# Performance work log

Hardware: AMD Instinct MI355X
Metric: run time of the kernel (lower is better)

## Reference

```python
import jax, jax.numpy as jnp
import numpy as np

B, SEQ, DIM = 4, 2048, 2048
NH, HD = 16, 128            # head_dim = dim // n_head
HID = 5632                  # int(2*(4*dim)/3) rounded up to multiple_of=256
EPS = 1e-5
THETA = 500000.0


def setup_inputs() -> dict:
    key = jax.random.key(0)
    ks = jax.random.split(key, 9)
    s = 0.02  # init scale keeps activations/logits well-conditioned
    x = jax.random.normal(ks[0], (B, SEQ, DIM), jnp.float32)
    wq = jax.random.normal(ks[1], (DIM, DIM), jnp.float32) * s
    wk = jax.random.normal(ks[2], (DIM, DIM), jnp.float32) * s
    wv = jax.random.normal(ks[3], (DIM, DIM), jnp.float32) * s
    wo = jax.random.normal(ks[4], (DIM, DIM), jnp.float32) * s
    w1 = jax.random.normal(ks[5], (DIM, HID), jnp.float32) * s
    w2 = jax.random.normal(ks[6], (HID, DIM), jnp.float32) * s
    w3 = jax.random.normal(ks[7], (DIM, HID), jnp.float32) * s
    attn_norm_w = jnp.ones((DIM,), jnp.float32)
    ffn_norm_w = jnp.ones((DIM,), jnp.float32)
    # RoPE tables (real/imag of freqs_cis), [seq, head_dim//2]
    inv = 1.0 / (THETA ** (jnp.arange(0, HD, 2, dtype=jnp.float32) / HD))
    ang = jnp.arange(SEQ, dtype=jnp.float32)[:, None] * inv[None, :]
    return dict(x=x, wq=wq, wk=wk, wv=wv, wo=wo, w1=w1, w2=w2, w3=w3,
                attn_norm_w=attn_norm_w, ffn_norm_w=ffn_norm_w,
                freqs_cos=jnp.cos(ang), freqs_sin=jnp.sin(ang))


def rmsnorm(x, w, eps=EPS):
    return x * jax.lax.rsqrt(jnp.mean(x * x, axis=-1, keepdims=True) + eps) * w


def rope(x, cos, sin):
    # x: [b, s, h, d]; pairs (d0,d1),(d2,d3),... treated as complex, multiplied by e^{i*ang}
    a, b = x[..., 0::2], x[..., 1::2]
    c = cos[None, :, None, :]
    s = sin[None, :, None, :]
    return jnp.stack([a * c - b * s, a * s + b * c], axis=-1).reshape(x.shape)


def block(x, wq, wk, wv, wo, w1, w2, w3, attn_norm_w, ffn_norm_w, freqs_cos, freqs_sin):
    b, s, d = x.shape
    # --- attention sublayer ---
    hn = rmsnorm(x, attn_norm_w)
    q = (hn @ wq).reshape(b, s, NH, HD)
    k = (hn @ wk).reshape(b, s, NH, HD)
    v = (hn @ wv).reshape(b, s, NH, HD)
    q = rope(q, freqs_cos, freqs_sin)
    k = rope(k, freqs_cos, freqs_sin)
    scores = jnp.einsum('bqhd,bkhd->bhqk', q, k) / np.float32(np.sqrt(HD))
    mask = jnp.triu(jnp.full((s, s), -jnp.inf, dtype=scores.dtype), k=1)
    p = jax.nn.softmax(scores + mask, axis=-1)
    attn = jnp.einsum('bhqk,bkhd->bqhd', p, v).reshape(b, s, d) @ wo
    h = x + attn
    # --- SwiGLU FFN sublayer ---
    fn = rmsnorm(h, ffn_norm_w)
    ffn = (jax.nn.silu(fn @ w1) * (fn @ w3)) @ w2
    return h + ffn


def reference(x, wq, wk, wv, wo, w1, w2, w3, attn_norm_w, ffn_norm_w, freqs_cos, freqs_sin):
    return block(x, wq, wk, wv, wo, w1, w2, w3, attn_norm_w, ffn_norm_w, freqs_cos, freqs_sin)
```

## Files before the change

### kernel.cpp

```cpp
#include <hip/hip_runtime.h>
#include <stdint.h>

#define DIMV 2048
#define SEQV 2048
#define NHV 16
#define HDV 128
#define HIDV 5632
#define NROWS 8192
#define LDP 6144

typedef short bf16x8 __attribute__((ext_vector_type(8)));
typedef float f32x4 __attribute__((ext_vector_type(4)));
typedef unsigned short u16x8 __attribute__((ext_vector_type(8)));

#define GLD16(src, dst) __builtin_amdgcn_global_load_lds( \
    (const __attribute__((address_space(1))) unsigned int*)(src), \
    (__attribute__((address_space(3))) unsigned int*)(dst), 16, 0, 0)

__device__ __forceinline__ float bf2f(unsigned short u){
  union { unsigned u; float f; } x; x.u = ((unsigned)u) << 16; return x.f;
}
__device__ __forceinline__ unsigned short f2bf(float f){
  union { float f; unsigned u; } x; x.f = f;
  unsigned r = x.u + 0x7fffu + ((x.u >> 16) & 1u);
  return (unsigned short)(r >> 16);
}

__global__ void transpose_cast4(const float* s0, const float* s1, const float* s2, const float* s3,
                                unsigned short* d0g, unsigned short* d1g, unsigned short* d2g, unsigned short* d3g,
                                int R, int C){
  __shared__ alignas(16) unsigned short tile[32][33];
  const float* in; unsigned short* out;
  switch (blockIdx.z){
    case 0: in = s0; out = d0g; break;
    case 1: in = s1; out = d1g; break;
    case 2: in = s2; out = d2g; break;
    default: in = s3; out = d3g; break;
  }
  int c0 = blockIdx.x * 32, r0 = blockIdx.y * 32;
  int tx = threadIdx.x, ty = threadIdx.y;
#pragma unroll
  for (int i = 0; i < 32; i += 8)
    tile[ty + i][tx] = f2bf(in[(long)(r0 + ty + i) * C + (c0 + tx)]);
  __syncthreads();
#pragma unroll
  for (int i = 0; i < 32; i += 8)
    out[(long)(c0 + ty + i) * R + (r0 + tx)] = tile[tx][ty + i];
}

__global__ void transpose_v(const unsigned short* __restrict__ packed, unsigned short* __restrict__ vt){
  __shared__ alignas(16) unsigned short tile[32][33];
  int bh = blockIdx.z;
  int b = bh >> 4, h = bh & 15;
  int d0 = blockIdx.y * 32, s0 = blockIdx.x * 32;
  int tx = threadIdx.x, ty = threadIdx.y;
  const unsigned short* src = packed + (long)b * SEQV * LDP + 4096 + (long)h * HDV;
  unsigned short* dst = vt + (long)bh * HDV * SEQV;
#pragma unroll
  for (int i = 0; i < 32; i += 8)
    tile[ty + i][tx] = src[(long)(s0 + ty + i) * LDP + d0 + tx];
  __syncthreads();
#pragma unroll
  for (int i = 0; i < 32; i += 8)
    dst[(long)(d0 + ty + i) * SEQV + s0 + tx] = tile[tx][ty + i];
}

__global__ __launch_bounds__(256) void rmsnorm_k(const float* __restrict__ x,
                                                 const float* __restrict__ w,
                                                 unsigned short* __restrict__ out){
  int row = blockIdx.x, t = threadIdx.x;
  const float* xr = x + (long)row * DIMV;
  float4 v0 = ((const float4*)xr)[t * 2];
  float4 v1 = ((const float4*)xr)[t * 2 + 1];
  float ss = v0.x*v0.x + v0.y*v0.y + v0.z*v0.z + v0.w*v0.w
           + v1.x*v1.x + v1.y*v1.y + v1.z*v1.z + v1.w*v1.w;
#pragma unroll
  for (int off = 32; off; off >>= 1) ss += __shfl_down(ss, off);
  __shared__ float red[4];
  if ((t & 63) == 0) red[t >> 6] = ss;
  __syncthreads();
  float tot = red[0] + red[1] + red[2] + red[3];
  float sc = rsqrtf(tot * (1.0f / DIMV) + 1e-5f);
  const float* wr = w + t * 8;
  float vv[8] = {v0.x, v0.y, v0.z, v0.w, v1.x, v1.y, v1.z, v1.w};
  u16x8 o;
#pragma unroll
  for (int e = 0; e < 8; e++) o[e] = f2bf(vv[e] * sc * wr[e]);
  *(u16x8*)(out + (long)row * DIMV + t * 8) = o;
}

#define SCHEDB() __builtin_amdgcn_sched_barrier(0)
#define SBAR()   __builtin_amdgcn_s_barrier()

template <int MODE>
__global__ __launch_bounds__(512, 2) void gemm256(const unsigned short* __restrict__ A, int lda,
                                                  const unsigned short* __restrict__ Bt,
                                                  unsigned short* __restrict__ Cb,
                                                  float* __restrict__ Cf,
                                                  const float* __restrict__ resid,
                                                  int ldc, int M, int N, int K){
  __shared__ alignas(16) unsigned short As[2][256 * 64];
  __shared__ alignas(16) unsigned short Bs[2][256 * 64];
  int m0 = blockIdx.y * 256, n0 = blockIdx.x * 256;
  int tid = threadIdx.x, w = tid >> 6, l = tid & 63;
  int wm = w >> 2, wn = w & 3;
  int l15 = l & 15, l4 = l >> 4;
  int sr8 = l >> 3, sl = l & 7;
  int nt = K / 64;

  f32x4 acc[8][4];
#pragma unroll
  for (int i = 0; i < 8; i++)
#pragma unroll
    for (int j = 0; j < 4; j++) acc[i][j] = (f32x4){0.f, 0.f, 0.f, 0.f};

#define GSTAGE(Gp, ld_, r0_, slab) { \
    _Pragma("unroll") \
    for (int r = 0; r < 2; r++){ \
      int row = (r * 8 + w) * 8 + sr8; \
      int cs = sl ^ (row & 7); \
      GLD16((Gp) + (long)((r0_) + row) * (ld_) + cs * 8, (slab) + (r * 8 + w) * 512); \
    } }
#define STAGE_A(tt, half) { int _t = (tt); if (_t < nt) GSTAGE(A + _t * 64, lda, m0 + (half) * 128, &As[_t & 1][(half) * 8192]) }
#define STAGE_B(tt, half) { int _t = (tt); if (_t < nt) GSTAGE(Bt + _t * 64, K, n0 + (half) * 128, &Bs[_t & 1][(half) * 8192]) }
#define LDA8(mi, ks) (*(const bf16x8*)(&As[bi][(wm * 128 + (mi) * 16 + l15) * 64 + (((ks) * 4 + l4) ^ (l15 & 7)) * 8]))
#define LDB8(ni, ks) (*(const bf16x8*)(&Bs[bi][(wn * 64 + (ni) * 16 + l15) * 64 + (((ks) * 4 + l4) ^ (l15 & 7)) * 8]))
#define MFMA4x2(AF, BF, MOFF, NOFF) { \
    _Pragma("unroll") \
    for (int mi = 0; mi < 4; mi++) \
      _Pragma("unroll") \
      for (int ni = 0; ni < 2; ni++) \
        _Pragma("unroll") \
        for (int ks = 0; ks < 2; ks++) \
          acc[mi + (MOFF)][ni + (NOFF)] = __builtin_amdgcn_mfma_f32_16x16x32_bf16(AF[mi][ks], BF[ni][ks], acc[mi + (MOFF)][ni + (NOFF)], 0, 0, 0); }

  STAGE_A(0, 0); STAGE_A(0, 1); STAGE_B(0, 0); STAGE_B(0, 1);
  STAGE_A(1, 0); STAGE_A(1, 1);
  asm volatile("s_waitcnt vmcnt(4)" ::: "memory");
  __syncthreads();

  for (int t = 0; t < nt; t++){
    int bi = t & 1;
    bf16x8 a03[4][2], a47[4][2], b01[2][2], b23[2][2];
#pragma unroll
    for (int mi = 0; mi < 4; mi++){ a03[mi][0] = LDA8(mi, 0); a03[mi][1] = LDA8(mi, 1); }
#pragma unroll
    for (int ni = 0; ni < 2; ni++){ b01[ni][0] = LDB8(ni, 0); b01[ni][1] = LDB8(ni, 1); }
    STAGE_B(t + 1, 0);
    SBAR();
    asm volatile("s_waitcnt lgkmcnt(0)" ::: "memory");
    SCHEDB();
    __builtin_amdgcn_s_setprio(1);
    MFMA4x2(a03, b01, 0, 0);
    __builtin_amdgcn_s_setprio(0);
    SBAR();
#pragma unroll
    for (int mi = 0; mi < 4; mi++){ a47[mi][0] = LDA8(mi + 4, 0); a47[mi][1] = LDA8(mi + 4, 1); }
    STAGE_B(t + 1, 1);
    SBAR();
    asm volatile("s_waitcnt lgkmcnt(0)" ::: "memory");
    SCHEDB();
    __builtin_amdgcn_s_setprio(1);
    MFMA4x2(a47, b01, 4, 0);
    __builtin_amdgcn_s_setprio(0);
    SBAR();
#pragma unroll
    for (int ni = 0; ni < 2; ni++){ b23[ni][0] = LDB8(ni + 2, 0); b23[ni][1] = LDB8(ni + 2, 1); }
    STAGE_A(t + 2, 0);
    SBAR();
    asm volatile("s_waitcnt lgkmcnt(0)" ::: "memory");
    SCHEDB();
    __builtin_amdgcn_s_setprio(1);
    MFMA4x2(a03, b23, 0, 2);
    __builtin_amdgcn_s_setprio(0);
    SBAR();
    STAGE_A(t + 2, 1);
    SBAR();
    __builtin_amdgcn_s_setprio(1);
    MFMA4x2(a47, b23, 4, 2);
    __builtin_amdgcn_s_setprio(0);
    if (t + 2 < nt) asm volatile("s_waitcnt vmcnt(4)" ::: "memory");
    else            asm volatile("s_waitcnt vmcnt(0)" ::: "memory");
    SBAR();
  }
#undef GSTAGE
#undef STAGE_A
#undef STAGE_B
#undef LDA8
#undef LDB8
#undef MFMA4x2

#pragma unroll
  for (int mi = 0; mi < 8; mi++)
#pragma unroll
    for (int ni = 0; ni < 4; ni++)
#pragma unroll
      for (int r = 0; r < 4; r++){
        int row = m0 + wm * 128 + mi * 16 + l4 * 4 + r;
        int col = n0 + wn * 64 + ni * 16 + l15;
        long idx = (long)row * ldc + col;
        float v = acc[mi][ni][r];
        if (MODE == 0) Cb[idx] = f2bf(v);
        else           Cf[idx] = v + resid[idx];
      }
}

__global__ __launch_bounds__(512, 2) void ffn13_256(const unsigned short* __restrict__ A,
                                                    const unsigned short* __restrict__ B1t,
                                                    const unsigned short* __restrict__ B3t,
                                                    unsigned short* __restrict__ G,
                                                    int M, int N, int K){
  __shared__ alignas(16) unsigned short As[2][256 * 64];
  __shared__ alignas(16) unsigned short B1s[2][128 * 64];
  __shared__ alignas(16) unsigned short B3s[2][128 * 64];
  int m0 = blockIdx.y * 256, n0 = blockIdx.x * 128;
  int tid = threadIdx.x, w = tid >> 6, l = tid & 63;
  int wm = w >> 2, wn = w & 3;
  int l15 = l & 15, l4 = l >> 4;
  int sr8 = l >> 3, sl = l & 7;
  int nt = K / 64;

  f32x4 acc1[8][2], acc3[8][2];
#pragma unroll
  for (int i = 0; i < 8; i++)
#pragma unroll
    for (int j = 0; j < 2; j++){ acc1[i][j] = (f32x4){0.f,0.f,0.f,0.f}; acc3[i][j] = (f32x4){0.f,0.f,0.f,0.f}; }

#define GSTAGE(Gp, ld_, r0_, slab) { \
    _Pragma("unroll") \
    for (int r = 0; r < 2; r++){ \
      int row = (r * 8 + w) * 8 + sr8; \
      int cs = sl ^ (row & 7); \
      GLD16((Gp) + (long)((r0_) + row) * (ld_) + cs * 8, (slab) + (r * 8 + w) * 512); \
    } }
#define STAGE_A(tt, half) { int _t = (tt); if (_t < nt) GSTAGE(A + _t * 64, K, m0 + (half) * 128, &As[_t & 1][(half) * 8192]) }
#define STAGE_B1(tt) { int _t = (tt); if (_t < nt) GSTAGE(B1t + _t * 64, K, n0, &B1s[_t & 1][0]) }
#define STAGE_B3(tt) { int _t = (tt); if (_t < nt) GSTAGE(B3t + _t * 64, K, n0, &B3s[_t & 1][0]) }
#define LDA8(mi, ks) (*(const bf16x8*)(&As[bi][(wm * 128 + (mi) * 16 + l15) * 64 + (((ks) * 4 + l4) ^ (l15 & 7)) * 8]))
#define LDB18(ni, ks) (*(const bf16x8*)(&B1s[bi][(wn * 32 + (ni) * 16 + l15) * 64 + (((ks) * 4 + l4) ^ (l15 & 7)) * 8]))
#define LDB38(ni, ks) (*(const bf16x8*)(&B3s[bi][(wn * 32 + (ni) * 16 + l15) * 64 + (((ks) * 4 + l4) ^ (l15 & 7)) * 8]))
#define MFMA4x2(AF, BF, ACC, MOFF) { \
    _Pragma("unroll") \
    for (int mi = 0; mi < 4; mi++) \
      _Pragma("unroll") \
      for (int ni = 0; ni < 2; ni++) \
        _Pragma("unroll") \
        for (int ks = 0; ks < 2; ks++) \
          ACC[mi + (MOFF)][ni] = __builtin_amdgcn_mfma_f32_16x16x32_bf16(AF[mi][ks], BF[ni][ks], ACC[mi + (MOFF)][ni], 0, 0, 0); }

  STAGE_A(0, 0); STAGE_A(0, 1); STAGE_B1(0); STAGE_B3(0);
  STAGE_A(1, 0); STAGE_A(1, 1);
  asm volatile("s_waitcnt vmcnt(4)" ::: "memory");
  __syncthreads();

  for (int t = 0; t < nt; t++){
    int bi = t & 1;
    bf16x8 a03[4][2], a47[4][2], b1f[2][2], b3f[2][2];
#pragma unroll
    for (int mi = 0; mi < 4; mi++){ a03[mi][0] = LDA8(mi, 0); a03[mi][1] = LDA8(mi, 1); }
#pragma unroll
    for (int ni = 0; ni < 2; ni++){ b1f[ni][0] = LDB18(ni, 0); b1f[ni][1] = LDB18(ni, 1); }
    STAGE_B1(t + 1);
    SBAR();
    asm volatile("s_waitcnt lgkmcnt(0)" ::: "memory");
    SCHEDB();
    __builtin_amdgcn_s_setprio(1);
    MFMA4x2(a03, b1f, acc1, 0);
    __builtin_amdgcn_s_setprio(0);
    SBAR();
#pragma unroll
    for (int mi = 0; mi < 4; mi++){ a47[mi][0] = LDA8(mi + 4, 0); a47[mi][1] = LDA8(mi + 4, 1); }
    STAGE_B3(t + 1);
    SBAR();
    asm volatile("s_waitcnt lgkmcnt(0)" ::: "memory");
    SCHEDB();
    __builtin_amdgcn_s_setprio(1);
    MFMA4x2(a47, b1f, acc1, 4);
    __builtin_amdgcn_s_setprio(0);
    SBAR();
#pragma unroll
    for (int ni = 0; ni < 2; ni++){ b3f[ni][0] = LDB38(ni, 0); b3f[ni][1] = LDB38(ni, 1); }
    STAGE_A(t + 2, 0);
    SBAR();
    asm volatile("s_waitcnt lgkmcnt(0)" ::: "memory");
    SCHEDB();
    __builtin_amdgcn_s_setprio(1);
    MFMA4x2(a03, b3f, acc3, 0);
    __builtin_amdgcn_s_setprio(0);
    SBAR();
    STAGE_A(t + 2, 1);
    SBAR();
    __builtin_amdgcn_s_setprio(1);
    MFMA4x2(a47, b3f, acc3, 4);
    __builtin_amdgcn_s_setprio(0);
    if (t + 2 < nt) asm volatile("s_waitcnt vmcnt(4)" ::: "memory");
    else            asm volatile("s_waitcnt vmcnt(0)" ::: "memory");
    SBAR();
  }
#undef GSTAGE
#undef STAGE_A
#undef STAGE_B1
#undef STAGE_B3
#undef LDA8
#undef LDB18
#undef LDB38
#undef MFMA4x2

#pragma unroll
  for (int mi = 0; mi < 8; mi++)
#pragma unroll
    for (int ni = 0; ni < 2; ni++)
#pragma unroll
      for (int r = 0; r < 4; r++){
        int row = m0 + wm * 128 + mi * 16 + l4 * 4 + r;
        int col = n0 + wn * 32 + ni * 16 + l15;
        float a = acc1[mi][ni][r];
        float si = a * (1.f / (1.f + __expf(-a)));
        G[(long)row * N + col] = f2bf(si * acc3[mi][ni][r]);
      }
}

__global__ __launch_bounds__(256) void rope_k(unsigned short* __restrict__ p,
                                              const float* __restrict__ cosT,
                                              const float* __restrict__ sinT,
                                              float qscale){
  long idx = (long)blockIdx.x * 256 + threadIdx.x;
  int i = (int)(idx & 63);
  long t = idx >> 6;
  int h = (int)(t & 15);
  long row = t >> 4;
  int s = (int)(row & (SEQV - 1));
  float c = cosT[s * 64 + i], sn = sinT[s * 64 + i];
  long base = row * LDP + h * HDV + 2 * i;
  unsigned pq = *(unsigned*)(p + base);
  float a = bf2f((unsigned short)(pq & 0xffff)), b = bf2f((unsigned short)(pq >> 16));
  float ra = (a * c - b * sn) * qscale, rb = (a * sn + b * c) * qscale;
  *(unsigned*)(p + base) = (unsigned)f2bf(ra) | ((unsigned)f2bf(rb) << 16);
  unsigned pk = *(unsigned*)(p + base + 2048);
  a = bf2f((unsigned short)(pk & 0xffff)); b = bf2f((unsigned short)(pk >> 16));
  ra = a * c - b * sn; rb = a * sn + b * c;
  *(unsigned*)(p + base + 2048) = (unsigned)f2bf(ra) | ((unsigned)f2bf(rb) << 16);
}

__global__ __launch_bounds__(512) void attn_k(unsigned short* __restrict__ p,
                                              const unsigned short* __restrict__ vt){
  __shared__ alignas(16) unsigned short Ks[2][64 * 128];
  __shared__ alignas(16) unsigned short Vs[2][128 * 64];
  __shared__ alignas(16) unsigned short Ps[8][16 * 64];
  int qt = (gridDim.x - 1) - blockIdx.x;
  int bh = blockIdx.y;
  int b = bh >> 4, h = bh & 15;
  int tid = threadIdx.x, w = tid >> 6, l = tid & 63;
  int l15 = l & 15, l4 = l >> 4;
  int qrow0 = qt * 128 + w * 16;
  long baseQ = (long)b * SEQV * LDP + (long)h * HDV;
  long baseV = (long)bh * HDV * SEQV;

  bf16x8 qf[4];
#pragma unroll
  for (int dc = 0; dc < 4; dc++)
    qf[dc] = *(const bf16x8*)(p + baseQ + (long)(qrow0 + l15) * LDP + dc * 32 + l4 * 8);

  f32x4 acc[8];
#pragma unroll
  for (int df = 0; df < 8; df++) acc[df] = (f32x4){0.f, 0.f, 0.f, 0.f};
  float mOld[4], lsum[4];
#pragma unroll
  for (int r = 0; r < 4; r++){ mOld[r] = -1e30f; lsum[r] = 0.f; }

#define ATTN_STAGE(buf, kt) {                                                       \
    int k0 = (kt) * 64;                                                             \
    _Pragma("unroll")                                                               \
    for (int i = 0; i < 2; i++){                                                    \
      int row = w * 8 + i * 4 + (l >> 4);                                           \
      int slot = (l & 15) ^ (row & 7);                                              \
      GLD16(p + baseQ + 2048 + (long)(k0 + row) * LDP + slot * 8,                   \
            Ks[buf] + (w * 8 + i * 4) * 128);                                       \
    }                                                                               \
    _Pragma("unroll")                                                               \
    for (int i = 0; i < 2; i++){                                                    \
      int row = w * 16 + i * 8 + (l >> 3);                                          \
      int slot = (l & 7) ^ (row & 7);                                               \
      GLD16(vt + baseV + (long)row * SEQV + k0 + slot * 8,                          \
            Vs[buf] + (w * 16 + i * 8) * 64);                                       \
    } }

  int ntile = 2 * (qt + 1);
  ATTN_STAGE(0, 0);
  asm volatile("s_waitcnt vmcnt(0)" ::: "memory");
  __syncthreads();
  int cur = 0;
  for (int tki = 0; tki < ntile; tki++){
    int k0 = tki * 64;
    if (tki + 1 < ntile) ATTN_STAGE(cur ^ 1, tki + 1);

    float s[4][4];
    __builtin_amdgcn_s_setprio(1);
#pragma unroll
    for (int kf = 0; kf < 4; kf++){
      f32x4 sf = (f32x4){0.f, 0.f, 0.f, 0.f};
#pragma unroll
      for (int dc = 0; dc < 4; dc++){
        bf16x8 kb = *(const bf16x8*)(Ks[cur] + (kf * 16 + l15) * 128 + (((dc * 4 + l4) ^ (l15 & 7)) * 8));
        sf = __builtin_amdgcn_mfma_f32_16x16x32_bf16(qf[dc], kb, sf, 0, 0, 0);
      }
      int key = k0 + kf * 16 + l15;
#pragma unroll
      for (int r = 0; r < 4; r++){
        int rowi = qrow0 + l4 * 4 + r;
        s[kf][r] = (key <= rowi) ? sf[r] : -1e30f;
      }
    }
    __builtin_amdgcn_s_setprio(0);
    float scale[4];
#pragma unroll
    for (int r = 0; r < 4; r++){
      float vmax = fmaxf(fmaxf(s[0][r], s[1][r]), fmaxf(s[2][r], s[3][r]));
      for (int mm = 8; mm; mm >>= 1) vmax = fmaxf(vmax, __shfl_xor(vmax, mm));
      float mNew = fmaxf(mOld[r], vmax);
      scale[r] = __expf(mOld[r] - mNew);
      float ps = 0.f;
#pragma unroll
      for (int kf = 0; kf < 4; kf++){
        float pp = __expf(s[kf][r] - mNew);
        s[kf][r] = pp;
        ps += pp;
      }
      for (int mm = 8; mm; mm >>= 1) ps += __shfl_xor(ps, mm);
      lsum[r] = lsum[r] * scale[r] + ps;
      mOld[r] = mNew;
    }
#pragma unroll
    for (int df = 0; df < 8; df++)
#pragma unroll
      for (int r = 0; r < 4; r++) acc[df][r] *= scale[r];
#pragma unroll
    for (int kf = 0; kf < 4; kf++)
#pragma unroll
      for (int r = 0; r < 4; r++){
        int row = l4 * 4 + r;
        int sidx = row * 64 + (((((kf * 16 + l15) * 2)) ^ ((row & 7) << 4)) >> 1);
        Ps[w][sidx] = f2bf(s[kf][r]);
      }
    __builtin_amdgcn_s_setprio(1);
#pragma unroll
    for (int kc = 0; kc < 2; kc++){
      bf16x8 pa = *(const bf16x8*)(Ps[w] + l15 * 64 + (((kc * 64 + l4 * 16) ^ ((l15 & 7) << 4)) >> 1));
#pragma unroll
      for (int df = 0; df < 8; df++){
        bf16x8 vb = *(const bf16x8*)(Vs[cur] + (df * 16 + l15) * 64 + (((kc * 4 + l4) ^ (l15 & 7)) * 8));
        acc[df] = __builtin_amdgcn_mfma_f32_16x16x32_bf16(pa, vb, acc[df], 0, 0, 0);
      }
    }
    __builtin_amdgcn_s_setprio(0);
    asm volatile("s_waitcnt vmcnt(0)" ::: "memory");
    __syncthreads();
    cur ^= 1;
  }
#pragma unroll
  for (int df = 0; df < 8; df++)
#pragma unroll
    for (int r = 0; r < 4; r++){
      int rows = qrow0 + l4 * 4 + r;
      p[baseQ + (long)rows * LDP + df * 16 + l15] = f2bf(acc[df][r] / lsum[r]);
    }
#undef ATTN_STAGE
}

extern "C" void kernel_launch(void* const* d_in, const int* in_sizes, int n_in,
                              void* d_out, int out_size, void* d_ws, size_t ws_size,
                              hipStream_t stream){
  const float* x    = (const float*)d_in[0];
  const float* wq   = (const float*)d_in[1];
  const float* wk   = (const float*)d_in[2];
  const float* wv   = (const float*)d_in[3];
  const float* wo   = (const float*)d_in[4];
  const float* w1   = (const float*)d_in[5];
  const float* w2   = (const float*)d_in[6];
  const float* w3   = (const float*)d_in[7];
  const float* anw  = (const float*)d_in[8];
  const float* fnw  = (const float*)d_in[9];
  const float* fcos = (const float*)d_in[10];
  const float* fsin = (const float*)d_in[11];

  char* ws = (char*)d_ws;
  size_t off = 0;
  auto alloc = [&](size_t bytes) -> void* {
    void* p = ws + off;
    off += (bytes + 255) & ~(size_t)255;
    return p;
  };
  const size_t SQ = (size_t)DIMV * DIMV * 2;
  const size_t SW = (size_t)DIMV * HIDV * 2;
  const size_t SA = (size_t)NROWS * DIMV * 2;
  const size_t SP = (size_t)NROWS * LDP * 2;

  unsigned short* wqT = (unsigned short*)alloc(SQ);
  unsigned short* wkT = (unsigned short*)alloc(SQ);
  unsigned short* wvT = (unsigned short*)alloc(SQ);
  unsigned short* woT = (unsigned short*)alloc(SQ);
  unsigned short* w1T = (unsigned short*)alloc(SW);
  unsigned short* w3T = (unsigned short*)alloc(SW);
  unsigned short* w2T = (unsigned short*)alloc(SW);
  unsigned short* hn  = (unsigned short*)alloc(SA);
  unsigned short* pk  = (unsigned short*)alloc(SP);
  unsigned short* vtb = hn;
  unsigned short* g   = pk;
  float* hf = (float*)d_out;
  (void)ws_size; (void)in_sizes; (void)n_in; (void)out_size;
  (void)wkT; (void)wvT;

  dim3 tb(32, 8);
  transpose_cast4<<<dim3(DIMV/32, DIMV/32, 4), tb, 0, stream>>>(wq, wk, wv, wo, wqT, wkT, wvT, woT, DIMV, DIMV);
  transpose_cast4<<<dim3(HIDV/32, DIMV/32, 2), tb, 0, stream>>>(w1, w3, nullptr, nullptr, w1T, w3T, nullptr, nullptr, DIMV, HIDV);
  transpose_cast4<<<dim3(DIMV/32, HIDV/32, 1), tb, 0, stream>>>(w2, nullptr, nullptr, nullptr, w2T, nullptr, nullptr, nullptr, HIDV, DIMV);

  rmsnorm_k<<<NROWS, 256, 0, stream>>>(x, anw, hn);

  gemm256<0><<<dim3(LDP/256, NROWS/256), 512, 0, stream>>>(hn, DIMV, wqT, pk, nullptr, nullptr, LDP, NROWS, LDP, DIMV);

  rope_k<<<(NROWS * NHV * 64) / 256, 256, 0, stream>>>(pk, fcos, fsin, 0.08838834764831845f);

  transpose_v<<<dim3(SEQV/32, HDV/32, 4 * NHV), tb, 0, stream>>>(pk, vtb);

  attn_k<<<dim3(SEQV/128, 4 * NHV), 512, 0, stream>>>(pk, vtb);

  gemm256<1><<<dim3(DIMV/256, NROWS/256), 512, 0, stream>>>(pk, LDP, woT, nullptr, hf, x, DIMV, NROWS, DIMV, DIMV);

  rmsnorm_k<<<NROWS, 256, 0, stream>>>(hf, fnw, hn);

  ffn13_256<<<dim3(HIDV/128, NROWS/256), 512, 0, stream>>>(hn, w1T, w3T, g, NROWS, HIDV, DIMV);

  gemm256<1><<<dim3(DIMV/256, NROWS/256), 512, 0, stream>>>(g, HIDV, w2T, nullptr, hf, (const float*)hf, DIMV, NROWS, DIMV, HIDV);
}
```

Before: 1.253 ms.

## Switch GEMM and FFN13 kernels from 16x16x32 to 32x32x16 bf16 MFMA tiles

Replaces the 16x16x32 MFMA instructions in both the generic 256x256 GEMM and the fused w1/w3 SwiGLU kernel with 32x32x16 MFMAs. LDS fragment loads, accumulator layout (f32x16) and the epilogue row/column mapping are rewritten to match the larger tile. Bigger MFMA tiles need fewer LDS fragment reads per FLOP and issue fewer instructions. The cost is a different swizzle access pattern that may cause LDS bank conflicts, and the same register pressure.

```diff
diff --git a/kernel.cpp b/kernel.cpp
--- a/kernel.cpp
+++ b/kernel.cpp
@@ -11,6 +11,7 @@
 
 typedef short bf16x8 __attribute__((ext_vector_type(8)));
 typedef float f32x4 __attribute__((ext_vector_type(4)));
+typedef float f32x16 __attribute__((ext_vector_type(16)));
 typedef unsigned short u16x8 __attribute__((ext_vector_type(8)));
 
 #define GLD16(src, dst) __builtin_amdgcn_global_load_lds( \
@@ -104,15 +105,17 @@
   int m0 = blockIdx.y * 256, n0 = blockIdx.x * 256;
   int tid = threadIdx.x, w = tid >> 6, l = tid & 63;
   int wm = w >> 2, wn = w & 3;
-  int l15 = l & 15, l4 = l >> 4;
+  int l31 = l & 31, l5 = l >> 5;
   int sr8 = l >> 3, sl = l & 7;
   int nt = K / 64;
 
-  f32x4 acc[8][4];
-#pragma unroll
-  for (int i = 0; i < 8; i++)
-#pragma unroll
-    for (int j = 0; j < 4; j++) acc[i][j] = (f32x4){0.f, 0.f, 0.f, 0.f};
+  f32x16 acc[4][2];
+#pragma unroll
+  for (int i = 0; i < 4; i++)
+#pragma unroll
+    for (int j = 0; j < 2; j++)
+#pragma unroll
+      for (int e = 0; e < 16; e++) acc[i][j][e] = 0.f;
 
 #define GSTAGE(Gp, ld_, r0_, slab) { \
     _Pragma("unroll") \
@@ -123,16 +126,15 @@
     } }
 #define STAGE_A(tt, half) { int _t = (tt); if (_t < nt) GSTAGE(A + _t * 64, lda, m0 + (half) * 128, &As[_t & 1][(half) * 8192]) }
 #define STAGE_B(tt, half) { int _t = (tt); if (_t < nt) GSTAGE(Bt + _t * 64, K, n0 + (half) * 128, &Bs[_t & 1][(half) * 8192]) }
-#define LDA8(mi, ks) (*(const bf16x8*)(&As[bi][(wm * 128 + (mi) * 16 + l15) * 64 + (((ks) * 4 + l4) ^ (l15 & 7)) * 8]))
-#define LDB8(ni, ks) (*(const bf16x8*)(&Bs[bi][(wn * 64 + (ni) * 16 + l15) * 64 + (((ks) * 4 + l4) ^ (l15 & 7)) * 8]))
-#define MFMA4x2(AF, BF, MOFF, NOFF) { \
+#define LDA32(mb, ks) (*(const bf16x8*)(&As[bi][(wm * 128 + (mb) * 32 + l31) * 64 + (((ks) * 2 + l5) ^ (l31 & 7)) * 8]))
+#define LDB32(nb, ks) (*(const bf16x8*)(&Bs[bi][(wn * 64 + (nb) * 32 + l31) * 64 + (((ks) * 2 + l5) ^ (l31 & 7)) * 8]))
+#define MFMA_Q(AF, NB, MOFF) { \
     _Pragma("unroll") \
-    for (int mi = 0; mi < 4; mi++) \
+    for (int ks = 0; ks < 4; ks++) \
       _Pragma("unroll") \
-      for (int ni = 0; ni < 2; ni++) \
-        _Pragma("unroll") \
-        for (int ks = 0; ks < 2; ks++) \
-          acc[mi + (MOFF)][ni + (NOFF)] = __builtin_amdgcn_mfma_f32_16x16x32_bf16(AF[mi][ks], BF[ni][ks], acc[mi + (MOFF)][ni + (NOFF)], 0, 0, 0); }
+      for (int mb = 0; mb < 2; mb++) \
+        acc[mb + (MOFF)][NB] = __builtin_amdgcn_mfma_f32_32x32x16_bf16(AF[mb][ks], \
+            (NB) ? b1[ks] : b0[ks], acc[mb + (MOFF)][NB], 0, 0, 0); }
 
   STAGE_A(0, 0); STAGE_A(0, 1); STAGE_B(0, 0); STAGE_B(0, 1);
   STAGE_A(1, 0); STAGE_A(1, 1);
@@ -141,43 +143,47 @@
 
   for (int t = 0; t < nt; t++){
     int bi = t & 1;
-    bf16x8 a03[4][2], a47[4][2], b01[2][2], b23[2][2];
-#pragma unroll
-    for (int mi = 0; mi < 4; mi++){ a03[mi][0] = LDA8(mi, 0); a03[mi][1] = LDA8(mi, 1); }
-#pragma unroll
-    for (int ni = 0; ni < 2; ni++){ b01[ni][0] = LDB8(ni, 0); b01[ni][1] = LDB8(ni, 1); }
+    bf16x8 a01[2][4], a23[2][4], b0[4], b1[4];
+#pragma unroll
+    for (int mb = 0; mb < 2; mb++)
+#pragma unroll
+      for (int ks = 0; ks < 4; ks++) a01[mb][ks] = LDA32(mb, ks);
+#pragma unroll
+    for (int ks = 0; ks < 4; ks++) b0[ks] = LDB32(0, ks);
     STAGE_B(t + 1, 0);
     SBAR();
     asm volatile("s_waitcnt lgkmcnt(0)" ::: "memory");
     SCHEDB();
     __builtin_amdgcn_s_setprio(1);
-    MFMA4x2(a03, b01, 0, 0);
-    __builtin_amdgcn_s_setprio(0);
-    SBAR();
-#pragma unroll
-    for (int mi = 0; mi < 4; mi++){ a47[mi][0] = LDA8(mi + 4, 0); a47[mi][1] = LDA8(mi + 4, 1); }
+    MFMA_Q(a01, 0, 0);
+    __builtin_amdgcn_s_setprio(0);
+    SBAR();
+#pragma unroll
+    for (int mb = 0; mb < 2; mb++)
+#pragma unroll
+      for (int ks = 0; ks < 4; ks++) a23[mb][ks] = LDA32(mb + 2, ks);
     STAGE_B(t + 1, 1);
     SBAR();
     asm volatile("s_waitcnt lgkmcnt(0)" ::: "memory");
     SCHEDB();
     __builtin_amdgcn_s_setprio(1);
-    MFMA4x2(a47, b01, 4, 0);
-    __builtin_amdgcn_s_setprio(0);
-    SBAR();
-#pragma unroll
-    for (int ni = 0; ni < 2; ni++){ b23[ni][0] = LDB8(ni + 2, 0); b23[ni][1] = LDB8(ni + 2, 1); }
+    MFMA_Q(a23, 0, 2);
+    __builtin_amdgcn_s_setprio(0);
+    SBAR();
+#pragma unroll
+    for (int ks = 0; ks < 4; ks++) b1[ks] = LDB32(1, ks);
     STAGE_A(t + 2, 0);
     SBAR();
     asm volatile("s_waitcnt lgkmcnt(0)" ::: "memory");
     SCHEDB();
     __builtin_amdgcn_s_setprio(1);
-    MFMA4x2(a03, b23, 0, 2);
+    MFMA_Q(a01, 1, 0);
     __builtin_amdgcn_s_setprio(0);
     SBAR();
     STAGE_A(t + 2, 1);
     SBAR();
     __builtin_amdgcn_s_setprio(1);
-    MFMA4x2(a47, b23, 4, 2);
+    MFMA_Q(a23, 1, 2);
     __builtin_amdgcn_s_setprio(0);
     if (t + 2 < nt) asm volatile("s_waitcnt vmcnt(4)" ::: "memory");
     else            asm volatile("s_waitcnt vmcnt(0)" ::: "memory");
@@ -186,20 +192,20 @@
 #undef GSTAGE
 #undef STAGE_A
 #undef STAGE_B
-#undef LDA8
-#undef LDB8
-#undef MFMA4x2
-
-#pragma unroll
-  for (int mi = 0; mi < 8; mi++)
-#pragma unroll
-    for (int ni = 0; ni < 4; ni++)
-#pragma unroll
-      for (int r = 0; r < 4; r++){
-        int row = m0 + wm * 128 + mi * 16 + l4 * 4 + r;
-        int col = n0 + wn * 64 + ni * 16 + l15;
+#undef LDA32
+#undef LDB32
+#undef MFMA_Q
+
+#pragma unroll
+  for (int mb = 0; mb < 4; mb++)
+#pragma unroll
+    for (int nb = 0; nb < 2; nb++)
+#pragma unroll
+      for (int rg = 0; rg < 16; rg++){
+        int row = m0 + wm * 128 + mb * 32 + (rg & 3) + ((rg >> 2) << 3) + (l5 << 2);
+        int col = n0 + wn * 64 + nb * 32 + l31;
         long idx = (long)row * ldc + col;
-        float v = acc[mi][ni][r];
+        float v = acc[mb][nb][rg];
         if (MODE == 0) Cb[idx] = f2bf(v);
         else           Cf[idx] = v + resid[idx];
       }
@@ -216,15 +222,15 @@
   int m0 = blockIdx.y * 256, n0 = blockIdx.x * 128;
   int tid = threadIdx.x, w = tid >> 6, l = tid & 63;
   int wm = w >> 2, wn = w & 3;
-  int l15 = l & 15, l4 = l >> 4;
+  int l31 = l & 31, l5 = l >> 5;
   int sr8 = l >> 3, sl = l & 7;
   int nt = K / 64;
 
-  f32x4 acc1[8][2], acc3[8][2];
-#pragma unroll
-  for (int i = 0; i < 8; i++)
-#pragma unroll
-    for (int j = 0; j < 2; j++){ acc1[i][j] = (f32x4){0.f,0.f,0.f,0.f}; acc3[i][j] = (f32x4){0.f,0.f,0.f,0.f}; }
+  f32x16 acc1[4], acc3[4];
+#pragma unroll
+  for (int i = 0; i < 4; i++)
+#pragma unroll
+    for (int e = 0; e < 16; e++){ acc1[i][e] = 0.f; acc3[i][e] = 0.f; }
 
 #define GSTAGE(Gp, ld_, r0_, slab) { \
     _Pragma("unroll") \
@@ -236,17 +242,15 @@
 #define STAGE_A(tt, half) { int _t = (tt); if (_t < nt) GSTAGE(A + _t * 64, K, m0 + (half) * 128, &As[_t & 1][(half) * 8192]) }
 #define STAGE_B1(tt) { int _t = (tt); if (_t < nt) GSTAGE(B1t + _t * 64, K, n0, &B1s[_t & 1][0]) }
 #define STAGE_B3(tt) { int _t = (tt); if (_t < nt) GSTAGE(B3t + _t * 64, K, n0, &B3s[_t & 1][0]) }
-#define LDA8(mi, ks) (*(const bf16x8*)(&As[bi][(wm * 128 + (mi) * 16 + l15) * 64 + (((ks) * 4 + l4) ^ (l15 & 7)) * 8]))
-#define LDB18(ni, ks) (*(const bf16x8*)(&B1s[bi][(wn * 32 + (ni) * 16 + l15) * 64 + (((ks) * 4 + l4) ^ (l15 & 7)) * 8]))
-#define LDB38(ni, ks) (*(const bf16x8*)(&B3s[bi][(wn * 32 + (ni) * 16 + l15) * 64 + (((ks) * 4 + l4) ^ (l15 & 7)) * 8]))
-#define MFMA4x2(AF, BF, ACC, MOFF) { \
+#define LDA32(mb, ks) (*(const bf16x8*)(&As[bi][(wm * 128 + (mb) * 32 + l31) * 64 + (((ks) * 2 + l5) ^ (l31 & 7)) * 8]))
+#define LDB132(ks) (*(const bf16x8*)(&B1s[bi][(wn * 32 + l31) * 64 + (((ks) * 2 + l5) ^ (l31 & 7)) * 8]))
+#define LDB332(ks) (*(const bf16x8*)(&B3s[bi][(wn * 32 + l31) * 64 + (((ks) * 2 + l5) ^ (l31 & 7)) * 8]))
+#define MFMA_Q(AF, BF, ACC, MOFF) { \
     _Pragma("unroll") \
-    for (int mi = 0; mi < 4; mi++) \
+    for (int ks = 0; ks < 4; ks++) \
       _Pragma("unroll") \
-      for (int ni = 0; ni < 2; ni++) \
-        _Pragma("unroll") \
-        for (int ks = 0; ks < 2; ks++) \
-          ACC[mi + (MOFF)][ni] = __builtin_amdgcn_mfma_f32_16x16x32_bf16(AF[mi][ks], BF[ni][ks], ACC[mi + (MOFF)][ni], 0, 0, 0); }
+      for (int mb = 0; mb < 2; mb++) \
+        ACC[mb + (MOFF)] = __builtin_amdgcn_mfma_f32_32x32x16_bf16(AF[mb][ks], BF[ks], ACC[mb + (MOFF)], 0, 0, 0); }
 
   STAGE_A(0, 0); STAGE_A(0, 1); STAGE_B1(0); STAGE_B3(0);
   STAGE_A(1, 0); STAGE_A(1, 1);
@@ -255,43 +259,47 @@
 
   for (int t = 0; t < nt; t++){
     int bi = t & 1;
-    bf16x8 a03[4][2], a47[4][2], b1f[2][2], b3f[2][2];
-#pragma unroll
-    for (int mi = 0; mi < 4; mi++){ a03[mi][0] = LDA8(mi, 0); a03[mi][1] = LDA8(mi, 1); }
-#pragma unroll
-    for (int ni = 0; ni < 2; ni++){ b1f[ni][0] = LDB18(ni, 0); b1f[ni][1] = LDB18(ni, 1); }
+    bf16x8 a01[2][4], a23[2][4], b1f[4], b3f[4];
+#pragma unroll
+    for (int mb = 0; mb < 2; mb++)
+#pragma unroll
+      for (int ks = 0; ks < 4; ks++) a01[mb][ks] = LDA32(mb, ks);
+#pragma unroll
+    for (int ks = 0; ks < 4; ks++) b1f[ks] = LDB132(ks);
     STAGE_B1(t + 1);
     SBAR();
     asm volatile("s_waitcnt lgkmcnt(0)" ::: "memory");
     SCHEDB();
     __builtin_amdgcn_s_setprio(1);
-    MFMA4x2(a03, b1f, acc1, 0);
-    __builtin_amdgcn_s_setprio(0);
-    SBAR();
-#pragma unroll
-    for (int mi = 0; mi < 4; mi++){ a47[mi][0] = LDA8(mi + 4, 0); a47[mi][1] = LDA8(mi + 4, 1); }
+    MFMA_Q(a01, b1f, acc1, 0);
+    __builtin_amdgcn_s_setprio(0);
+    SBAR();
+#pragma unroll
+    for (int mb = 0; mb < 2; mb++)
+#pragma unroll
+      for (int ks = 0; ks < 4; ks++) a23[mb][ks] = LDA32(mb + 2, ks);
     STAGE_B3(t + 1);
     SBAR();
     asm volatile("s_waitcnt lgkmcnt(0)" ::: "memory");
     SCHEDB();
     __builtin_amdgcn_s_setprio(1);
-    MFMA4x2(a47, b1f, acc1, 4);
-    __builtin_amdgcn_s_setprio(0);
-    SBAR();
-#pragma unroll
-    for (int ni = 0; ni < 2; ni++){ b3f[ni][0] = LDB38(ni, 0); b3f[ni][1] = LDB38(ni, 1); }
+    MFMA_Q(a23, b1f, acc1, 2);
+    __builtin_amdgcn_s_setprio(0);
+    SBAR();
+#pragma unroll
+    for (int ks = 0; ks < 4; ks++) b3f[ks] = LDB332(ks);
     STAGE_A(t + 2, 0);
     SBAR();
     asm volatile("s_waitcnt lgkmcnt(0)" ::: "memory");
     SCHEDB();
     __builtin_amdgcn_s_setprio(1);
-    MFMA4x2(a03, b3f, acc3, 0);
+    MFMA_Q(a01, b3f, acc3, 0);
     __builtin_amdgcn_s_setprio(0);
     SBAR();
     STAGE_A(t + 2, 1);
     SBAR();
     __builtin_amdgcn_s_setprio(1);
-    MFMA4x2(a47, b3f, acc3, 4);
+    MFMA_Q(a23, b3f, acc3, 2);
     __builtin_amdgcn_s_setprio(0);
     if (t + 2 < nt) asm volatile("s_waitcnt vmcnt(4)" ::: "memory");
     else            asm volatile("s_waitcnt vmcnt(0)" ::: "memory");
@@ -301,23 +309,21 @@
 #undef STAGE_A
 #undef STAGE_B1
 #undef STAGE_B3
-#undef LDA8
-#undef LDB18
-#undef LDB38
-#undef MFMA4x2
-
-#pragma unroll
-  for (int mi = 0; mi < 8; mi++)
-#pragma unroll
-    for (int ni = 0; ni < 2; ni++)
-#pragma unroll
-      for (int r = 0; r < 4; r++){
-        int row = m0 + wm * 128 + mi * 16 + l4 * 4 + r;
-        int col = n0 + wn * 32 + ni * 16 + l15;
-        float a = acc1[mi][ni][r];
-        float si = a * (1.f / (1.f + __expf(-a)));
-        G[(long)row * N + col] = f2bf(si * acc3[mi][ni][r]);
-      }
+#undef LDA32
+#undef LDB132
+#undef LDB332
+#undef MFMA_Q
+
+#pragma unroll
+  for (int mb = 0; mb < 4; mb++)
+#pragma unroll
+    for (int rg = 0; rg < 16; rg++){
+      int row = m0 + wm * 128 + mb * 32 + (rg & 3) + ((rg >> 2) << 3) + (l5 << 2);
+      int col = n0 + wn * 32 + l31;
+      float a = acc1[mb][rg];
+      float si = a * (1.f / (1.f + __expf(-a)));
+      G[(long)row * N + col] = f2bf(si * acc3[mb][rg]);
+    }
 }
 
 __global__ __launch_bounds__(256) void rope_k(unsigned short* __restrict__ p,
```

Result: slower. 1.351 ms (+7.8%).
